# Kernel optimization log

Hardware: AMD Instinct MI355X
Metric: run time of the kernel (lower is better)

## Reference

```python
import jax, jax.numpy as jnp
import numpy as np

B, C = 8, 2048          # batch, out_dim (projection channels)
HG = WG = 32            # global crop feature map
HL = WL = 12            # local crop feature map
STUDENT_TEMP = 0.1
TEMP_SCHEDULE = np.concatenate([np.linspace(0.04, 0.07, 30), np.ones(100 - 30) * 0.07])

# Fixed relative boxes (x1, x2, y1, y2) per (iq, v) crop pair, shared across the
# batch so grid shapes are static. Source computes grid_H from teacher_feat.shape[0]
# (= C, a quirk of the original code) and grid_W from shape[1] (= spatial H); boxes
# are chosen so resulting grids are ~[22-25, 22-24].
PAIRS = [
    (0, 1, (-0.80, 0.70, -0.500, -0.475), (-0.90, 0.60, -0.60, 0.60)),
    (0, 2, (-0.75, 0.75,  0.100,  0.125), (-0.80, 0.80, -0.80, 0.80)),
    (0, 3, (-0.60, 0.90, -0.200, -0.178), (-0.70, 0.90, -0.90, 0.70)),
    (1, 0, (-0.70, 0.80,  0.300,  0.322), (-0.85, 0.65, -0.50, 0.90)),
    (1, 2, (-0.90, 0.50, -0.100, -0.076), (-0.60, 0.95, -0.95, 0.60)),
    (1, 3, (-0.50, 0.95,  0.200,  0.224), (-0.90, 0.90, -0.40, 0.95)),
]


def _grid_dims(box, Hc, Wc):
    x1, x2, y1, y2 = box
    return int(abs(y1 - y2) / 2 * Hc), int(abs(x1 - x2) / 2 * Wc)  # (grid_H, grid_W)


def _make_grid(box, gH, gW):
    # Faithful to source: meshgrid([linspace(y1,y2,gH), linspace(x1,x2,gW)]),
    # stacked so channel 0 holds the y-linspace (which grid_sample reads as x).
    x1, x2, y1, y2 = box
    yy, xx = jnp.meshgrid(jnp.linspace(y1, y2, gH), jnp.linspace(x1, x2, gW), indexing='ij')
    return jnp.stack([yy, xx], axis=-1)  # [gH, gW, 2]


def _grid_sample_border(img, grid):
    # torch.nn.functional.grid_sample, bilinear, padding_mode='border',
    # align_corners=False. img: [B, C, H, W], grid: [gH, gW, 2] (same grid per batch).
    H, W = img.shape[-2], img.shape[-1]
    gx, gy = grid[..., 0], grid[..., 1]
    ix = jnp.clip((gx + 1.0) * (W * 0.5) - 0.5, 0.0, W - 1.0)  # border: clip coords
    iy = jnp.clip((gy + 1.0) * (H * 0.5) - 0.5, 0.0, H - 1.0)
    x0f, y0f = jnp.floor(ix), jnp.floor(iy)
    wx = (ix - x0f)[None, None]  # [1,1,gH,gW]
    wy = (iy - y0f)[None, None]
    x0 = x0f.astype(jnp.int32)
    y0 = y0f.astype(jnp.int32)
    x1 = jnp.minimum(x0 + 1, W - 1)
    y1 = jnp.minimum(y0 + 1, H - 1)
    v00 = img[:, :, y0, x0]
    v01 = img[:, :, y0, x1]
    v10 = img[:, :, y1, x0]
    v11 = img[:, :, y1, x1]
    return (1.0 - wy) * ((1.0 - wx) * v00 + wx * v01) + wy * ((1.0 - wx) * v10 + wx * v11)


def setup_inputs() -> dict:
    key = jax.random.key(0)
    ks = jax.random.split(key, 7)
    return {
        'student_g0': jax.random.normal(ks[0], (B, C, HG, WG), jnp.float32),
        'student_g1': jax.random.normal(ks[1], (B, C, HG, WG), jnp.float32),
        'student_l0': jax.random.normal(ks[2], (B, C, HL, WL), jnp.float32),
        'student_l1': jax.random.normal(ks[3], (B, C, HL, WL), jnp.float32),
        'teacher_g0': jax.random.normal(ks[4], (B, C, HG, WG), jnp.float32),
        'teacher_g1': jax.random.normal(ks[5], (B, C, HG, WG), jnp.float32),
        'center': jax.random.normal(ks[6], (1, C), jnp.float32) * 0.1,
        'epoch': 5,
    }


def reference(student_g0, student_g1, student_l0, student_l1,
              teacher_g0, teacher_g1, center, epoch):
    temp = float(TEMP_SCHEDULE[epoch])
    students = [s / STUDENT_TEMP for s in (student_g0, student_g1, student_l0, student_l1)]
    cen = center[:, :, None, None]  # [1,C,1,1]
    cteach = [jax.nn.softmax((t - cen) / temp, axis=1) for t in (teacher_g0, teacher_g1)]

    losses = []
    for iq, v, tbox, sbox in PAIRS:
        tfeat = cteach[iq]   # [B,C,H,W]
        sfeat = students[v]  # [B,C,h,w]
        # Faithful: source passes (shape[0]=C, shape[1]=spatial H) as (H, W).
        gH, gW = _grid_dims(tbox, C, tfeat.shape[2])
        t_common = jax.lax.stop_gradient(_grid_sample_border(tfeat, _make_grid(tbox, gH, gW)))
        s_common = _grid_sample_border(sfeat, _make_grid(sbox, gH, gW))
        # cross-entropy over channels -> [B, gH, gW]
        loss = (-t_common * jax.nn.log_softmax(s_common, axis=1)).sum(axis=1)
        losses.append(loss.reshape(-1))
    return jnp.concatenate(losses).mean()
```

## Files before the change

### kernel.cpp

```cpp
#include <hip/hip_runtime.h>
#include <hip/hip_fp16.h>

#define NPOS 26688

struct PairInfo {
  int iq, v, Hs, gH, gW, base, per;
  unsigned magicPer, magicW;
  int tOfs, tN, tCb;
  int sN, sCb;
  float tx1, tx2, ty1, ty2;
  float sx1, sx2, sy1, sy2;
};

__constant__ PairInfo g_pairs[6] = {
  {0,1,32,25,24,    0,600, 7158279u,178956971u,    0,2, 7, 22,5, -0.80f,0.70f,-0.500f,-0.475f,  -0.90f,0.60f,-0.60f,0.60f},
  {0,2,12,25,24, 4800,600, 7158279u,178956971u,  512,2,17, 12,0, -0.75f,0.75f, 0.100f, 0.125f,  -0.80f,0.80f,-0.80f,0.80f},
  {0,3,12,22,24, 9600,528, 8134408u,178956971u, 1024,2,12, 12,0, -0.60f,0.90f,-0.200f,-0.178f,  -0.70f,0.90f,-0.90f,0.70f},
  {1,0,32,22,24,13824,528, 8134408u,178956971u, 1536,2,20, 24,7, -0.70f,0.80f, 0.300f, 0.322f,  -0.85f,0.65f,-0.50f,0.90f},
  {1,2,12,24,22,18048,528, 8134408u,195225787u, 2048,3,13, 12,0, -0.90f,0.50f,-0.100f,-0.076f,  -0.60f,0.95f,-0.95f,0.60f},
  {1,3,12,24,23,22272,552, 7780739u,186737709u, 2816,3,18, 12,0, -0.50f,0.95f, 0.200f, 0.224f,  -0.90f,0.90f,-0.40f,0.95f},
};

__constant__ int g_ux[2][32] = {
  {-1,-1,-1,-1,-1,-1,-1, 0, 1,-1,-1,-1, 2, 3,-1,-1,-1, 4, 5,-1,-1,-1,-1,-1,-1,-1,-1,-1,-1,-1,-1,-1},
  {-1,-1,-1,-1,-1,-1,-1,-1,-1,-1,-1,-1,-1, 0, 1, 2,-1,-1, 3, 4, 5, 6,-1,-1,-1,-1,-1,-1,-1,-1,-1,-1},
};
__constant__ int g_weSlot[2][8] = {{0,1,2,3,4,5,0,0},{0,1,2,3,4,5,5,6}};
__constant__ int g_weBase[2][8] = {{0,1,1024,1025,512,513,0,0},
                                   {2048,2049,2050,2816,2817,2818,1536,1537}};
__constant__ int g_weStr[2][8]  = {{2,2,2,2,2,2,2,2},{3,3,3,3,3,3,2,2}};
__constant__ int g_weN[2] = {6, 8};

__device__ inline float get_invtemp(const int* __restrict__ ep) {
  int e = ep[0];
  e = e < 0 ? 0 : (e > 99 ? 99 : e);
  float temp = (e < 30) ? (0.04f + (float)e * (0.03f / 29.0f)) : 0.07f;
  return 1.0f / temp;
}

typedef _Float16 hv2 __attribute__((ext_vector_type(2)));
__device__ inline float fdot2f(__half2 a, __half2 b, float c) {
#if defined(__has_builtin)
#if __has_builtin(__builtin_amdgcn_fdot2)
  return __builtin_amdgcn_fdot2(*reinterpret_cast<hv2*>(&a),
                                *reinterpret_cast<hv2*>(&b), c, false);
#else
  float2 af = __half22float2(a), bf = __half22float2(b);
  return fmaf(af.x, bf.x, fmaf(af.y, bf.y, c));
#endif
#else
  float2 af = __half22float2(a), bf = __half22float2(b);
  return fmaf(af.x, bf.x, fmaf(af.y, bf.y, c));
#endif
}

__global__ __launch_bounds__(256) void dino_phase1(
    const float* __restrict__ tg0, const float* __restrict__ tg1,
    float* __restrict__ Tcf,
    const float* __restrict__ sg0, const float* __restrict__ sg1,
    __half* __restrict__ Sg0, __half* __restrict__ Sg1,
    const float* __restrict__ sl0, const float* __restrict__ sl1,
    __half* __restrict__ Sl0, __half* __restrict__ Sl1) {
  __shared__ float smem[5700];
  int bid = blockIdx.x;
  int t = threadIdx.x;

  if (bid < 2048) {
    int cg = bid & 127;
    int b = (bid >> 7) & 7;
    int view = bid >> 10;
    const float* __restrict__ src = view ? tg1 : tg0;
    const float* base = src + ((size_t)(b * 2048 + cg * 16)) * 1024;
#pragma unroll
    for (int k = 0; k < 16; ++k) {
      int idx = k * 256 + t;
      int c = idx >> 8, p4 = idx & 255;
      int y = p4 >> 3, x0 = (p4 & 7) * 4;
      float4 v = *reinterpret_cast<const float4*>(base + (size_t)c * 1024 + p4 * 4);
      int s0 = g_ux[view][x0],     s1 = g_ux[view][x0 + 1];
      int s2 = g_ux[view][x0 + 2], s3 = g_ux[view][x0 + 3];
      if (s0 >= 0) smem[s0 * 544 + y * 17 + c] = v.x;
      if (s1 >= 0) smem[s1 * 544 + y * 17 + c] = v.y;
      if (s2 >= 0) smem[s2 * 544 + y * 17 + c] = v.z;
      if (s3 >= 0) smem[s3 * 544 + y * 17 + c] = v.w;
    }
    __syncthreads();
    int nw = g_weN[view];
    if (t < nw * 32) {
      int e = t >> 5, y = t & 31;
      int slot = g_weSlot[view][e];
      int tex = g_weBase[view][e] + (b * 32 + y) * g_weStr[view][e];
      tex = min(max(tex, 0), 3583);
      float arr[16];
#pragma unroll
      for (int c = 0; c < 16; ++c) arr[c] = smem[slot * 544 + y * 17 + c];
      float* dp = Tcf + (size_t)tex * 2048 + cg * 16;
#pragma unroll
      for (int q = 0; q < 4; ++q)
        *reinterpret_cast<float4*>(dp + q * 4) =
            make_float4(arr[4 * q], arr[4 * q + 1], arr[4 * q + 2], arr[4 * q + 3]);
    }
    return;
  }

  if (bid < 4096) {
    int lb = bid - 2048;
    int cg = lb & 127;
    int b = (lb >> 7) & 7;
    int which = lb >> 10;
    const float* __restrict__ src = which ? sg1 : sg0;
    __half* __restrict__ dst = which ? Sg1 : Sg0;
    int cb = which ? 5 : 7;
    int n = which ? 22 : 24;
    unsigned magicN = which ? 195225787u : 178956971u;
    const float* base = src + ((size_t)(b * 2048 + cg * 16)) * 1024;
    __half* hlds = reinterpret_cast<__half*>(smem);
#pragma unroll
    for (int k = 0; k < 16; ++k) {
      int idx = k * 256 + t;
      int c = idx >> 8, p4 = idx & 255;
      int y = p4 >> 3, x0 = (p4 & 7) * 4;
      float4 v = *reinterpret_cast<const float4*>(base + (size_t)c * 1024 + p4 * 4);
      if (y >= 1 && y <= 26) {
        int rb = (y - 1) * n - cb;
#pragma unroll
        for (int q = 0; q < 4; ++q) {
          int x = x0 + q;
          if (x >= cb && x < cb + n) {
            float val = (q == 0) ? v.x : (q == 1) ? v.y : (q == 2) ? v.z : v.w;
            hlds[(rb + x) * 18 + c] = __float2half(val * 10.f);
          }
        }
      }
    }
    __syncthreads();
    int total = 26 * n;
    const unsigned* hw = reinterpret_cast<const unsigned*>(smem);
#pragma unroll
    for (int k2 = 0; k2 < 3; ++k2) {
      int u = t + 256 * k2;
      if (u < total) {
        int yy = (int)__umulhi((unsigned)u, magicN);
        int cx = u - yy * n;
        int y = yy + 1;
        unsigned r[8];
#pragma unroll
        for (int q = 0; q < 8; ++q) r[q] = hw[u * 9 + q];
        unsigned* dp = reinterpret_cast<unsigned*>(
            dst + ((size_t)((b * 32 + y) * n + cx)) * 2048 + cg * 16);
        *reinterpret_cast<uint4*>(dp) = make_uint4(r[0], r[1], r[2], r[3]);
        *reinterpret_cast<uint4*>(dp + 4) = make_uint4(r[4], r[5], r[6], r[7]);
      }
    }
    return;
  }

  float* tile = smem;
  int lb = bid - 4096;
  int ct = lb & 127;
  int g = lb >> 7;
  int b = g & 7;
  int vv = g >> 3;
  const float* __restrict__ src = vv ? sl1 : sl0;
  __half* __restrict__ dst = vv ? Sl1 : Sl0;
  const float* sp = src + ((size_t)(b * 2048 + ct * 16)) * 144;
#pragma unroll
  for (int k = 0; k < 9; ++k) {
    int idx = t + 256 * k;
    int c = idx / 144;
    int yx = idx - c * 144;
    tile[c * 145 + yx] = sp[idx] * 10.f;
  }
  __syncthreads();
  __half* dp = dst + ((size_t)(b * 144)) * 2048 + ct * 16;
#pragma unroll
  for (int k = 0; k < 2; ++k) {
    int u = t + 256 * k;
    if (u < 288) {
      int yx = u >> 1, q8 = (u & 1) * 8;
      __half hv[8];
#pragma unroll
      for (int j = 0; j < 8; ++j) hv[j] = __float2half(tile[(q8 + j) * 145 + yx]);
      *reinterpret_cast<float4*>(dp + (size_t)yx * 2048 + q8) =
          *reinterpret_cast<float4*>(hv);
    }
  }
}

__global__ __launch_bounds__(256) void dino_probs(
    const float* __restrict__ Tcf, __half* __restrict__ Tp,
    const float* __restrict__ cen, const int* __restrict__ ep) {
  __shared__ float rm[4], rs[4];
  int tex = blockIdx.x;
  int t = threadIdx.x;
  int lane = t & 63, w = t >> 6;
  float invtemp = get_invtemp(ep);

  const float* cp = Tcf + (size_t)tex * 2048 + t * 8;
  float4 v0 = *reinterpret_cast<const float4*>(cp);
  float4 v1 = *reinterpret_cast<const float4*>(cp + 4);
  float4 c0 = *reinterpret_cast<const float4*>(cen + t * 8);
  float4 c1 = *reinterpret_cast<const float4*>(cen + t * 8 + 4);
  float lg[8];
  lg[0] = (v0.x - c0.x) * invtemp; lg[1] = (v0.y - c0.y) * invtemp;
  lg[2] = (v0.z - c0.z) * invtemp; lg[3] = (v0.w - c0.w) * invtemp;
  lg[4] = (v1.x - c1.x) * invtemp; lg[5] = (v1.y - c1.y) * invtemp;
  lg[6] = (v1.z - c1.z) * invtemp; lg[7] = (v1.w - c1.w) * invtemp;

  float m = lg[0];
#pragma unroll
  for (int q = 1; q < 8; ++q) m = fmaxf(m, lg[q]);
#pragma unroll
  for (int off = 32; off; off >>= 1) m = fmaxf(m, __shfl_xor(m, off));
  if (lane == 0) rm[w] = m;
  __syncthreads();
  float M = fmaxf(fmaxf(rm[0], rm[1]), fmaxf(rm[2], rm[3]));

  float e[8];
  float s = 0.f;
#pragma unroll
  for (int q = 0; q < 8; ++q) { e[q] = __expf(lg[q] - M); s += e[q]; }
#pragma unroll
  for (int off = 32; off; off >>= 1) s += __shfl_xor(s, off);
  if (lane == 0) rs[w] = s;
  __syncthreads();
  float invS = 1.f / (rs[0] + rs[1] + rs[2] + rs[3]);

  __half o[8];
#pragma unroll
  for (int q = 0; q < 8; ++q) o[q] = __float2half(e[q] * invS);
  *reinterpret_cast<uint4*>(Tp + (size_t)tex * 2048 + t * 8) =
      *reinterpret_cast<uint4*>(o);
}

union H8 { uint4 u; __half2 h[4]; };

__global__ __launch_bounds__(256) void dino_main(
    const __half* __restrict__ Tp,
    const __half* __restrict__ S0, const __half* __restrict__ S1,
    const __half* __restrict__ S2, const __half* __restrict__ S3,
    float* __restrict__ losses) {
  int wid = threadIdx.x >> 6, lane = threadIdx.x & 63;
  int pair = blockIdx.x / 1200;
  int slot = blockIdx.x - pair * 1200;
  PairInfo pi = g_pairs[pair];
  int posInPair = slot * 4 + wid;
  if (posInPair >= pi.per * 8) return;

  unsigned up = (unsigned)posInPair;
  int b = (int)__umulhi(up, pi.magicPer);
  b = min(max(b, 0), 7);
  int r = posInPair - b * pi.per;
  r = min(max(r, 0), pi.per - 1);
  int i = (int)__umulhi((unsigned)r, pi.magicW);
  i = min(max(i, 0), pi.gH - 1);
  int j = r - i * pi.gW;
  j = min(max(j, 0), pi.gW - 1);

  float tyy = pi.ty1 + (float)i * (pi.ty2 - pi.ty1) / (float)(pi.gH - 1);
  float txx = pi.tx1 + (float)j * (pi.tx2 - pi.tx1) / (float)(pi.gW - 1);
  float tix = fminf(fmaxf((tyy + 1.0f) * 16.0f - 0.5f, 0.0f), 31.0f);
  float tiy = fminf(fmaxf((txx + 1.0f) * 16.0f - 0.5f, 0.0f), 31.0f);
  int tx0 = (int)tix, ty0 = (int)tiy;
  float wxt = tix - (float)tx0, wyt = tiy - (float)ty0;
  int tx1i = min(tx0 + 1, 31), ty1i = min(ty0 + 1, 31);

  int hs = pi.Hs;
  float hh = 0.5f * (float)hs, hm = (float)(hs - 1);
  float syy = pi.sy1 + (float)i * (pi.sy2 - pi.sy1) / (float)(pi.gH - 1);
  float sxx = pi.sx1 + (float)j * (pi.sx2 - pi.sx1) / (float)(pi.gW - 1);
  float six = fminf(fmaxf((syy + 1.0f) * hh - 0.5f, 0.0f), hm);
  float siy = fminf(fmaxf((sxx + 1.0f) * hh - 0.5f, 0.0f), hm);
  int sx0 = (int)six, sy0 = (int)siy;
  float wxs = six - (float)sx0, wys = siy - (float)sy0;
  int sx1i = min(sx0 + 1, hs - 1), sy1i = min(sy0 + 1, hs - 1);

  const __half* __restrict__ S =
      (pi.v == 0) ? S0 : (pi.v == 1) ? S1 : (pi.v == 2) ? S2 : S3;

  int tc0 = min(max(tx0 - pi.tCb, 0), pi.tN - 1);
  int tc1 = min(max(tx1i - pi.tCb, 0), pi.tN - 1);
  int trow = pi.tOfs + (b * 32 + ty0) * pi.tN;
  int trow1 = pi.tOfs + (b * 32 + ty1i) * pi.tN;
  int toff00 = min(trow + tc0, 3583) * 2048;
  int toff01 = min(trow + tc1, 3583) * 2048;
  int toff10 = min(trow1 + tc0, 3583) * 2048;
  int toff11 = min(trow1 + tc1, 3583) * 2048;
  int sc0 = min(max(sx0 - pi.sCb, 0), pi.sN - 1);
  int sc1 = min(max(sx1i - pi.sCb, 0), pi.sN - 1);
  int soff00 = ((b * hs + sy0) * pi.sN + sc0) * 2048;
  int soff01 = ((b * hs + sy0) * pi.sN + sc1) * 2048;
  int soff10 = ((b * hs + sy1i) * pi.sN + sc0) * 2048;
  int soff11 = ((b * hs + sy1i) * pi.sN + sc1) * 2048;

  __half2 wt00 = __float2half2_rn((1.f - wyt) * (1.f - wxt));
  __half2 wt01 = __float2half2_rn((1.f - wyt) * wxt);
  __half2 wt10 = __float2half2_rn(wyt * (1.f - wxt));
  __half2 wt11 = __float2half2_rn(wyt * wxt);
  __half2 ws00 = __float2half2_rn((1.f - wys) * (1.f - wxs));
  __half2 ws01 = __float2half2_rn((1.f - wys) * wxs);
  __half2 ws10 = __float2half2_rn(wys * (1.f - wxs));
  __half2 ws11 = __float2half2_rn(wys * wxs);

  float sum = 0.f, dot = 0.f;
#pragma unroll
  for (int k = 0; k < 4; ++k) {
    int c0 = (k << 9) + (lane << 3);
    H8 t00, t01, t10, t11, a00, a01, a10, a11;
    t00.u = *reinterpret_cast<const uint4*>(Tp + toff00 + c0);
    t01.u = *reinterpret_cast<const uint4*>(Tp + toff01 + c0);
    t10.u = *reinterpret_cast<const uint4*>(Tp + toff10 + c0);
    t11.u = *reinterpret_cast<const uint4*>(Tp + toff11 + c0);
    a00.u = *reinterpret_cast<const uint4*>(S + soff00 + c0);
    a01.u = *reinterpret_cast<const uint4*>(S + soff01 + c0);
    a10.u = *reinterpret_cast<const uint4*>(S + soff10 + c0);
    a11.u = *reinterpret_cast<const uint4*>(S + soff11 + c0);
#pragma unroll
    for (int p = 0; p < 4; ++p) {
      __half2 tc2 = __hmul2(wt00, t00.h[p]);
      tc2 = __hfma2(wt01, t01.h[p], tc2);
      tc2 = __hfma2(wt10, t10.h[p], tc2);
      tc2 = __hfma2(wt11, t11.h[p], tc2);
      __half2 sc2 = __hmul2(ws00, a00.h[p]);
      sc2 = __hfma2(ws01, a01.h[p], sc2);
      sc2 = __hfma2(ws10, a10.h[p], sc2);
      sc2 = __hfma2(ws11, a11.h[p], sc2);
      dot = fdot2f(tc2, sc2, dot);
      float2 scf = __half22float2(sc2);
      sum += __expf(scf.x);
      sum += __expf(scf.y);
    }
  }
#pragma unroll
  for (int off = 32; off; off >>= 1) {
    sum += __shfl_down(sum, off);
    dot += __shfl_down(dot, off);
  }
  if (lane == 0) losses[pi.base + posInPair] = logf(sum) - dot;
}

__global__ __launch_bounds__(1024) void dino_reduce(const float* __restrict__ losses,
                                                    float* __restrict__ out) {
  __shared__ double sd[1024];
  int t = threadIdx.x;
  double a = 0.0;
  for (int i4 = t; i4 < 6672; i4 += 1024) {
    float4 v = *reinterpret_cast<const float4*>(losses + i4 * 4);
    a += (double)v.x + (double)v.y + (double)v.z + (double)v.w;
  }
  sd[t] = a;
  __syncthreads();
  for (int off = 512; off; off >>= 1) {
    if (t < off) sd[t] += sd[t + off];
    __syncthreads();
  }
  if (t == 0) out[0] = (float)(sd[0] / (double)NPOS);
}

extern "C" void kernel_launch(void* const* d_in, const int* in_sizes, int n_in,
                              void* d_out, int out_size, void* d_ws, size_t ws_size,
                              hipStream_t stream) {
  const float* sg0 = (const float*)d_in[0];
  const float* sg1 = (const float*)d_in[1];
  const float* sl0 = (const float*)d_in[2];
  const float* sl1 = (const float*)d_in[3];
  const float* tg0 = (const float*)d_in[4];
  const float* tg1 = (const float*)d_in[5];
  const float* cen = (const float*)d_in[6];
  const int* epoch = (const int*)d_in[7];
  float* out = (float*)d_out;
  char* w = (char*)d_ws;

  const size_t OFF_LOSS = 131072;
  const size_t OFF_TCF  = 262144;
  const size_t OFF_TP   = 29622272;
  const size_t OFF_SG0  = 44302336;
  const size_t OFF_SG1  = 69468160;
  const size_t OFF_SL0  = 92536832;
  const size_t OFF_SL1  = 97255424;

  float* losses = (float*)(w + OFF_LOSS);
  float* Tcf = (float*)(w + OFF_TCF);
  __half* Tp  = (__half*)(w + OFF_TP);
  __half* Sg0 = (__half*)(w + OFF_SG0);
  __half* Sg1 = (__half*)(w + OFF_SG1);
  __half* Sl0 = (__half*)(w + OFF_SL0);
  __half* Sl1 = (__half*)(w + OFF_SL1);

  dino_phase1<<<6144, 256, 0, stream>>>(tg0, tg1, Tcf, sg0, sg1, Sg0, Sg1,
                                        sl0, sl1, Sl0, Sl1);
  dino_probs<<<3584, 256, 0, stream>>>(Tcf, Tp, cen, epoch);
  dino_main<<<7200, 256, 0, stream>>>(Tp, Sg0, Sg1, Sl0, Sl1, losses);
  dino_reduce<<<1, 1024, 0, stream>>>(losses, out);
}
```

Baseline: 142.2 us.

## Store gathered teacher columns as fp16 and widen phase1 channel tiles

```diff
diff --git a/kernel.cpp b/kernel.cpp
--- a/kernel.cpp
+++ b/kernel.cpp
@@ -56,56 +56,56 @@
 
 __global__ __launch_bounds__(256) void dino_phase1(
     const float* __restrict__ tg0, const float* __restrict__ tg1,
-    float* __restrict__ Tcf,
+    __half* __restrict__ Tch,
     const float* __restrict__ sg0, const float* __restrict__ sg1,
     __half* __restrict__ Sg0, __half* __restrict__ Sg1,
     const float* __restrict__ sl0, const float* __restrict__ sl1,
     __half* __restrict__ Sl0, __half* __restrict__ Sl1) {
-  __shared__ float smem[5700];
+  __shared__ __half smem_h[11232];
   int bid = blockIdx.x;
   int t = threadIdx.x;
 
-  if (bid < 2048) {
-    int cg = bid & 127;
-    int b = (bid >> 7) & 7;
-    int view = bid >> 10;
+  if (bid < 1024) {
+    int cg = bid & 63;
+    int b = (bid >> 6) & 7;
+    int view = bid >> 9;
     const float* __restrict__ src = view ? tg1 : tg0;
-    const float* base = src + ((size_t)(b * 2048 + cg * 16)) * 1024;
-#pragma unroll
-    for (int k = 0; k < 16; ++k) {
-      int idx = k * 256 + t;
-      int c = idx >> 8, p4 = idx & 255;
-      int y = p4 >> 3, x0 = (p4 & 7) * 4;
-      float4 v = *reinterpret_cast<const float4*>(base + (size_t)c * 1024 + p4 * 4);
-      int s0 = g_ux[view][x0],     s1 = g_ux[view][x0 + 1];
-      int s2 = g_ux[view][x0 + 2], s3 = g_ux[view][x0 + 3];
-      if (s0 >= 0) smem[s0 * 544 + y * 17 + c] = v.x;
-      if (s1 >= 0) smem[s1 * 544 + y * 17 + c] = v.y;
-      if (s2 >= 0) smem[s2 * 544 + y * 17 + c] = v.z;
-      if (s3 >= 0) smem[s3 * 544 + y * 17 + c] = v.w;
+    const float* base = src + ((size_t)(b * 2048 + cg * 32)) * 1024;
+    int y = t >> 3, x0 = (t & 7) * 4;
+    int s0 = g_ux[view][x0], s1 = g_ux[view][x0 + 1];
+    int s2 = g_ux[view][x0 + 2], s3 = g_ux[view][x0 + 3];
+    int smax = max(max(s0, s1), max(s2, s3));
+    if (smax >= 0) {
+#pragma unroll 8
+      for (int c = 0; c < 32; ++c) {
+        float4 v = *reinterpret_cast<const float4*>(base + (size_t)c * 1024 + t * 4);
+        if (s0 >= 0) smem_h[s0 * 1280 + y * 40 + c] = __float2half(v.x);
+        if (s1 >= 0) smem_h[s1 * 1280 + y * 40 + c] = __float2half(v.y);
+        if (s2 >= 0) smem_h[s2 * 1280 + y * 40 + c] = __float2half(v.z);
+        if (s3 >= 0) smem_h[s3 * 1280 + y * 40 + c] = __float2half(v.w);
+      }
     }
     __syncthreads();
-    int nw = g_weN[view];
-    if (t < nw * 32) {
-      int e = t >> 5, y = t & 31;
-      int slot = g_weSlot[view][e];
-      int tex = g_weBase[view][e] + (b * 32 + y) * g_weStr[view][e];
-      tex = min(max(tex, 0), 3583);
-      float arr[16];
-#pragma unroll
-      for (int c = 0; c < 16; ++c) arr[c] = smem[slot * 544 + y * 17 + c];
-      float* dp = Tcf + (size_t)tex * 2048 + cg * 16;
-#pragma unroll
-      for (int q = 0; q < 4; ++q)
-        *reinterpret_cast<float4*>(dp + q * 4) =
-            make_float4(arr[4 * q], arr[4 * q + 1], arr[4 * q + 2], arr[4 * q + 3]);
+    int tasks = g_weN[view] * 128;
+#pragma unroll
+    for (int it = 0; it < 4; ++it) {
+      int u = t + it * 256;
+      if (u < tasks) {
+        int e = u >> 7, rem = u & 127, yy = rem >> 2, lq = rem & 3;
+        int slot = g_weSlot[view][e];
+        int tex = g_weBase[view][e] + (b * 32 + yy) * g_weStr[view][e];
+        tex = min(max(tex, 0), 3583);
+        uint4 val = *reinterpret_cast<const uint4*>(&smem_h[slot * 1280 + yy * 40 + lq * 8]);
+        *reinterpret_cast<uint4*>(Tch + (size_t)tex * 2048 + cg * 32 + lq * 8) = val;
+      }
     }
     return;
   }
 
-  if (bid < 4096) {
-    int lb = bid - 2048;
-    int cg = lb & 127;
+  if (bid < 3072) {
+    int lb = bid - 1024;
+    int cg = lb & 63;
+    int half = (lb >> 6) & 1;
     int b = (lb >> 7) & 7;
     int which = lb >> 10;
     const float* __restrict__ src = which ? sg1 : sg0;
@@ -113,82 +113,78 @@
     int cb = which ? 5 : 7;
     int n = which ? 22 : 24;
     unsigned magicN = which ? 195225787u : 178956971u;
-    const float* base = src + ((size_t)(b * 2048 + cg * 16)) * 1024;
-    __half* hlds = reinterpret_cast<__half*>(smem);
-#pragma unroll
-    for (int k = 0; k < 16; ++k) {
-      int idx = k * 256 + t;
-      int c = idx >> 8, p4 = idx & 255;
-      int y = p4 >> 3, x0 = (p4 & 7) * 4;
-      float4 v = *reinterpret_cast<const float4*>(base + (size_t)c * 1024 + p4 * 4);
-      if (y >= 1 && y <= 26) {
-        int rb = (y - 1) * n - cb;
-#pragma unroll
-        for (int q = 0; q < 4; ++q) {
-          int x = x0 + q;
-          if (x >= cb && x < cb + n) {
-            float val = (q == 0) ? v.x : (q == 1) ? v.y : (q == 2) ? v.z : v.w;
-            hlds[(rb + x) * 18 + c] = __float2half(val * 10.f);
-          }
-        }
+    int y0 = 1 + half * 13;
+    const float* pb = src + ((size_t)(b * 2048 + cg * 32)) * 1024 + y0 * 32;
+#pragma unroll 4
+    for (int it = 0; it < 13; ++it) {
+      int u2 = t + it * 256;
+      int c = u2 / 104;
+      int rem = u2 - c * 104;
+      int x0 = (rem & 7) * 4;
+      if (x0 + 3 >= cb && x0 < cb + n) {
+        float4 v = *reinterpret_cast<const float4*>(pb + (size_t)c * 1024 + rem * 4);
+        int pbase = (rem >> 3) * n - cb;
+        if (x0 >= cb && x0 < cb + n)         smem_h[(pbase + x0) * 36 + c] = __float2half(v.x * 10.f);
+        if (x0 + 1 >= cb && x0 + 1 < cb + n) smem_h[(pbase + x0 + 1) * 36 + c] = __float2half(v.y * 10.f);
+        if (x0 + 2 >= cb && x0 + 2 < cb + n) smem_h[(pbase + x0 + 2) * 36 + c] = __float2half(v.z * 10.f);
+        if (x0 + 3 >= cb && x0 + 3 < cb + n) smem_h[(pbase + x0 + 3) * 36 + c] = __float2half(v.w * 10.f);
       }
     }
     __syncthreads();
-    int total = 26 * n;
-    const unsigned* hw = reinterpret_cast<const unsigned*>(smem);
-#pragma unroll
-    for (int k2 = 0; k2 < 3; ++k2) {
-      int u = t + 256 * k2;
-      if (u < total) {
-        int yy = (int)__umulhi((unsigned)u, magicN);
-        int cx = u - yy * n;
-        int y = yy + 1;
-        unsigned r[8];
-#pragma unroll
-        for (int q = 0; q < 8; ++q) r[q] = hw[u * 9 + q];
-        unsigned* dp = reinterpret_cast<unsigned*>(
-            dst + ((size_t)((b * 32 + y) * n + cx)) * 2048 + cg * 16);
-        *reinterpret_cast<uint4*>(dp) = make_uint4(r[0], r[1], r[2], r[3]);
-        *reinterpret_cast<uint4*>(dp + 4) = make_uint4(r[4], r[5], r[6], r[7]);
+    int tasks = 13 * n * 4;
+#pragma unroll
+    for (int it = 0; it < 5; ++it) {
+      int u = t + it * 256;
+      if (u < tasks) {
+        int pos = u >> 2, lq = u & 3;
+        int yr = (int)__umulhi((unsigned)pos, magicN);
+        int cx = pos - yr * n;
+        int yy = y0 + yr;
+        uint2 a = *reinterpret_cast<const uint2*>(&smem_h[pos * 36 + lq * 8]);
+        uint2 b2 = *reinterpret_cast<const uint2*>(&smem_h[pos * 36 + lq * 8 + 4]);
+        *reinterpret_cast<uint4*>(dst + ((size_t)((b * 32 + yy) * n + cx)) * 2048 +
+                                  cg * 32 + lq * 8) = make_uint4(a.x, a.y, b2.x, b2.y);
       }
     }
     return;
   }
 
-  float* tile = smem;
-  int lb = bid - 4096;
-  int ct = lb & 127;
-  int g = lb >> 7;
-  int b = g & 7;
-  int vv = g >> 3;
+  int lb = bid - 3072;
+  int cg = lb & 63;
+  int b = (lb >> 6) & 7;
+  int vv = lb >> 9;
   const float* __restrict__ src = vv ? sl1 : sl0;
   __half* __restrict__ dst = vv ? Sl1 : Sl0;
-  const float* sp = src + ((size_t)(b * 2048 + ct * 16)) * 144;
-#pragma unroll
-  for (int k = 0; k < 9; ++k) {
-    int idx = t + 256 * k;
-    int c = idx / 144;
-    int yx = idx - c * 144;
-    tile[c * 145 + yx] = sp[idx] * 10.f;
+  const float* sp = src + ((size_t)(b * 2048 + cg * 32)) * 144;
+#pragma unroll
+  for (int it = 0; it < 5; ++it) {
+    int u = t + it * 256;
+    if (u < 1152) {
+      int c = u / 36;
+      int yx = (u - c * 36) * 4;
+      float4 v = *reinterpret_cast<const float4*>(sp + (size_t)u * 4);
+      smem_h[(yx + 0) * 36 + c] = __float2half(v.x * 10.f);
+      smem_h[(yx + 1) * 36 + c] = __float2half(v.y * 10.f);
+      smem_h[(yx + 2) * 36 + c] = __float2half(v.z * 10.f);
+      smem_h[(yx + 3) * 36 + c] = __float2half(v.w * 10.f);
+    }
   }
   __syncthreads();
-  __half* dp = dst + ((size_t)(b * 144)) * 2048 + ct * 16;
-#pragma unroll
-  for (int k = 0; k < 2; ++k) {
-    int u = t + 256 * k;
-    if (u < 288) {
-      int yx = u >> 1, q8 = (u & 1) * 8;
-      __half hv[8];
-#pragma unroll
-      for (int j = 0; j < 8; ++j) hv[j] = __float2half(tile[(q8 + j) * 145 + yx]);
-      *reinterpret_cast<float4*>(dp + (size_t)yx * 2048 + q8) =
-          *reinterpret_cast<float4*>(hv);
+#pragma unroll
+  for (int it = 0; it < 3; ++it) {
+    int u = t + it * 256;
+    if (u < 576) {
+      int pos = u >> 2, lq = u & 3;
+      uint2 a = *reinterpret_cast<const uint2*>(&smem_h[pos * 36 + lq * 8]);
+      uint2 b2 = *reinterpret_cast<const uint2*>(&smem_h[pos * 36 + lq * 8 + 4]);
+      *reinterpret_cast<uint4*>(dst + ((size_t)(b * 144 + pos)) * 2048 +
+                                cg * 32 + lq * 8) = make_uint4(a.x, a.y, b2.x, b2.y);
     }
   }
 }
 
 __global__ __launch_bounds__(256) void dino_probs(
-    const float* __restrict__ Tcf, __half* __restrict__ Tp,
+    const __half* __restrict__ Tch, __half* __restrict__ Tp,
     const float* __restrict__ cen, const int* __restrict__ ep) {
   __shared__ float rm[4], rs[4];
   int tex = blockIdx.x;
@@ -196,17 +192,19 @@
   int lane = t & 63, w = t >> 6;
   float invtemp = get_invtemp(ep);
 
-  const float* cp = Tcf + (size_t)tex * 2048 + t * 8;
-  float4 v0 = *reinterpret_cast<const float4*>(cp);
-  float4 v1 = *reinterpret_cast<const float4*>(cp + 4);
+  union { uint4 u; __half2 h[4]; } hv;
+  hv.u = *reinterpret_cast<const uint4*>(Tch + (size_t)tex * 2048 + t * 8);
   float4 c0 = *reinterpret_cast<const float4*>(cen + t * 8);
   float4 c1 = *reinterpret_cast<const float4*>(cen + t * 8 + 4);
   float lg[8];
-  lg[0] = (v0.x - c0.x) * invtemp; lg[1] = (v0.y - c0.y) * invtemp;
-  lg[2] = (v0.z - c0.z) * invtemp; lg[3] = (v0.w - c0.w) * invtemp;
-  lg[4] = (v1.x - c1.x) * invtemp; lg[5] = (v1.y - c1.y) * invtemp;
-  lg[6] = (v1.z - c1.z) * invtemp; lg[7] = (v1.w - c1.w) * invtemp;
-
+  {
+    float2 f0 = __half22float2(hv.h[0]), f1 = __half22float2(hv.h[1]);
+    float2 f2 = __half22float2(hv.h[2]), f3 = __half22float2(hv.h[3]);
+    lg[0] = (f0.x - c0.x) * invtemp; lg[1] = (f0.y - c0.y) * invtemp;
+    lg[2] = (f1.x - c0.z) * invtemp; lg[3] = (f1.y - c0.w) * invtemp;
+    lg[4] = (f2.x - c1.x) * invtemp; lg[5] = (f2.y - c1.y) * invtemp;
+    lg[6] = (f3.x - c1.z) * invtemp; lg[7] = (f3.y - c1.w) * invtemp;
+  }
   float m = lg[0];
 #pragma unroll
   for (int q = 1; q < 8; ++q) m = fmaxf(m, lg[q]);
@@ -372,24 +370,24 @@
   char* w = (char*)d_ws;
 
   const size_t OFF_LOSS = 131072;
-  const size_t OFF_TCF  = 262144;
-  const size_t OFF_TP   = 29622272;
-  const size_t OFF_SG0  = 44302336;
-  const size_t OFF_SG1  = 69468160;
-  const size_t OFF_SL0  = 92536832;
-  const size_t OFF_SL1  = 97255424;
+  const size_t OFF_TCH  = 262144;
+  const size_t OFF_TP   = 14942208;
+  const size_t OFF_SG0  = 29622272;
+  const size_t OFF_SG1  = 54788096;
+  const size_t OFF_SL0  = 77856768;
+  const size_t OFF_SL1  = 82575360;
 
   float* losses = (float*)(w + OFF_LOSS);
-  float* Tcf = (float*)(w + OFF_TCF);
+  __half* Tch = (__half*)(w + OFF_TCH);
   __half* Tp  = (__half*)(w + OFF_TP);
   __half* Sg0 = (__half*)(w + OFF_SG0);
   __half* Sg1 = (__half*)(w + OFF_SG1);
   __half* Sl0 = (__half*)(w + OFF_SL0);
   __half* Sl1 = (__half*)(w + OFF_SL1);
 
-  dino_phase1<<<6144, 256, 0, stream>>>(tg0, tg1, Tcf, sg0, sg1, Sg0, Sg1,
+  dino_phase1<<<4096, 256, 0, stream>>>(tg0, tg1, Tch, sg0, sg1, Sg0, Sg1,
                                         sl0, sl1, Sl0, Sl1);
-  dino_probs<<<3584, 256, 0, stream>>>(Tcf, Tp, cen, epoch);
+  dino_probs<<<3584, 256, 0, stream>>>(Tch, Tp, cen, epoch);
   dino_main<<<7200, 256, 0, stream>>>(Tp, Sg0, Sg1, Sl0, Sl1, losses);
   dino_reduce<<<1, 1024, 0, stream>>>(losses, out);
 }
```

Measured after the change: 122.0 us. 1.17x faster.
